# Kernel tuning notes

Measured on AMD Instinct MI355X. Metric: run time of the kernel, lower is better.

## Reference

```python
import jax, jax.numpy as jnp
import numpy as np

E = 1024      # embed_dim
H = 16        # num heads
D = E // H    # head_dim = 64
B, T = 4, 2048


def setup_inputs() -> dict:
    key = jax.random.key(0)
    ks = jax.random.split(key, 7)
    hidden_states = jax.random.normal(ks[0], (B, T, E), dtype=jnp.float32)
    # torch Linear weight layout: [out_features, in_features]
    Wqkv = jax.random.normal(ks[1], (3 * E, E), dtype=jnp.float32) * (1.0 / np.sqrt(E))
    bqkv = jax.random.normal(ks[2], (3 * E,), dtype=jnp.float32) * 0.02
    Wproj = jax.random.normal(ks[3], (E, E), dtype=jnp.float32) * (1.0 / np.sqrt(E))
    bproj = jax.random.normal(ks[4], (E,), dtype=jnp.float32) * 0.02
    splat_scale = jax.random.normal(ks[5], (H,), dtype=jnp.float32) * 0.5
    splat_bias = jax.random.normal(ks[6], (H, 1, 1), dtype=jnp.float32) * 0.5
    return {
        'hidden_states': hidden_states,
        'Wqkv': Wqkv, 'bqkv': bqkv,
        'Wproj': Wproj, 'bproj': bproj,
        'splat_scale': splat_scale, 'splat_bias': splat_bias,
    }


def reference(hidden_states, Wqkv, bqkv, Wproj, bproj, splat_scale, splat_bias):
    b, t, _ = hidden_states.shape
    scale_factor = 1.0 / np.sqrt(D)

    qkv = hidden_states @ Wqkv.T + bqkv                    # [B,T,3E]
    q, k, v = jnp.split(qkv, 3, axis=-1)
    # [B,H,T,D]
    q = q.reshape(b, t, H, D).transpose(0, 2, 1, 3)
    k = k.reshape(b, t, H, D).transpose(0, 2, 1, 3)
    v = v.reshape(b, t, H, D).transpose(0, 2, 1, 3)

    scores = jnp.einsum('bhqd,bhkd->bhqk', q * scale_factor, k)  # [B,H,T,T]

    s = (1.0 + 0.01 * jnp.tanh(splat_scale)).reshape(1, H, 1, 1)
    bsp = (0.001 * jnp.tanh(splat_bias)).reshape(1, H, 1, 1)
    scores = s * scores + bsp

    causal = jnp.tril(jnp.ones((t, t), dtype=bool))
    scores = jnp.where(causal, scores, jnp.float32(-1e9))

    attn = jax.nn.softmax(scores, axis=-1)                 # dropout = identity (eval)
    out = jnp.einsum('bhqk,bhkd->bhqd', attn, v)
    out = out.transpose(0, 2, 1, 3).reshape(b, t, E)
    out = out @ Wproj.T + bproj
    return out
```

## Files before the change

### kernel.cpp

```cpp
#include <hip/hip_runtime.h>
#include <stdint.h>

#define BB 4
#define TT 2048
#define EE 1024
#define HH 16
#define DD 64
#define MM (BB*TT)
#define NQKV (3*EE)

typedef __bf16 bf16_t;
typedef bf16_t bf16x8 __attribute__((ext_vector_type(8)));
typedef short  s16x4  __attribute__((ext_vector_type(4)));
typedef float  floatx4 __attribute__((ext_vector_type(4)));

__device__ __forceinline__ unsigned short f2bf(float f) {
    unsigned int u = __float_as_uint(f);
    u = (u + 0x7FFFu + ((u >> 16) & 1u)) >> 16;
    return (unsigned short)u;
}

__device__ __forceinline__ short bfs(float f) {
    return (short)__builtin_bit_cast(unsigned short, (bf16_t)f);
}

__device__ __forceinline__ void load_lds16(const void* g, void* l) {
    __builtin_amdgcn_global_load_lds(
        (const __attribute__((address_space(1))) unsigned int*)g,
        (__attribute__((address_space(3))) unsigned int*)l, 16, 0, 0);
}

__global__ void cvt_f32_bf16(const float* __restrict__ in,
                             unsigned short* __restrict__ out, int n) {
    int i = (blockIdx.x * 256 + threadIdx.x) * 4;
    if (i + 3 < n) {
        float4 v = *reinterpret_cast<const float4*>(in + i);
        ushort4 o;
        o.x = f2bf(v.x); o.y = f2bf(v.y); o.z = f2bf(v.z); o.w = f2bf(v.w);
        *reinterpret_cast<ushort4*>(out + i) = o;
    }
}

template<int N, int K, int EPI>
__global__ __launch_bounds__(256, 3) void gemm_bt(
    const unsigned short* __restrict__ A,
    const unsigned short* __restrict__ Bw,
    const float* __restrict__ bias,
    const float* __restrict__ sscale,
    unsigned short* __restrict__ Qb,
    unsigned short* __restrict__ Kb,
    unsigned short* __restrict__ Vtb,
    float* __restrict__ Cout)
{
    __shared__ __align__(16) unsigned short As[2][128 * 32];
    __shared__ __align__(16) unsigned short Bs[2][128 * 32];
    __shared__ float qsc[16];

    const int tid  = threadIdx.x;
    const int lane = tid & 63;
    const int w    = tid >> 6;
    const int quad = lane >> 4;
    const int l16  = lane & 15;
    const int m0   = blockIdx.y * 128;
    const int n0   = blockIdx.x * 128;
    const int wm   = (w & 1) * 64;
    const int wn   = (w >> 1) * 64;

    if (EPI == 0 && tid < 16) qsc[tid] = (1.0f + 0.01f * tanhf(sscale[tid])) * 0.125f;

    floatx4 acc[4][4] = {};

    const int rsl = (quad ^ ((l16 >> 1) & 3)) * 8;

    for (int kk = 0; kk < K; kk += 64) {
        __syncthreads();
#pragma unroll
        for (int h = 0; h < 2; ++h) {
#pragma unroll
            for (int c = 0; c < 2; ++c) {
                int idx = c * 256 + tid;
                int chk = (idx & 3) ^ ((idx >> 3) & 3);
                const unsigned short* ga = A  + (size_t)(m0 + (idx >> 2)) * K + kk + h * 32 + chk * 8;
                load_lds16(ga, &As[h][(c * 256 + w * 64) * 8]);
                const unsigned short* gb = Bw + (size_t)(n0 + (idx >> 2)) * K + kk + h * 32 + chk * 8;
                load_lds16(gb, &Bs[h][(c * 256 + w * 64) * 8]);
            }
        }
        __syncthreads();

#pragma unroll
        for (int h = 0; h < 2; ++h) {
            bf16x8 af[4], bfr[4];
#pragma unroll
            for (int mt = 0; mt < 4; ++mt)
                af[mt] = *reinterpret_cast<const bf16x8*>(&As[h][(wm + mt * 16 + l16) * 32 + rsl]);
#pragma unroll
            for (int nt = 0; nt < 4; ++nt)
                bfr[nt] = *reinterpret_cast<const bf16x8*>(&Bs[h][(wn + nt * 16 + l16) * 32 + rsl]);
#pragma unroll
            for (int mt = 0; mt < 4; ++mt)
#pragma unroll
                for (int nt = 0; nt < 4; ++nt)
                    acc[mt][nt] = __builtin_amdgcn_mfma_f32_16x16x32_bf16(af[mt], bfr[nt], acc[mt][nt], 0, 0, 0);
        }
    }

    if (EPI == 0) {
#pragma unroll
        for (int mt = 0; mt < 4; ++mt) {
            int rowb = m0 + wm + mt * 16 + quad * 4;
#pragma unroll
            for (int nt = 0; nt < 4; ++nt) {
                int col = n0 + wn + nt * 16 + l16;
                int which = col >> 10;
                int e = col & 1023;
                int h = e >> 6, d = e & 63;
                float bsv = bias[col];
#pragma unroll
                for (int r = 0; r < 4; ++r) {
                    int m = rowb + r;
                    int b = m >> 11, t = m & 2047;
                    float v = acc[mt][nt][r] + bsv;
                    size_t bh = (size_t)(b * HH + h);
                    if (which == 0) {
                        v *= qsc[h];
                        Qb[(bh * TT + t) * DD + d] = f2bf(v);
                    } else if (which == 1) {
                        Kb[(bh * TT + t) * DD + d] = f2bf(v);
                    } else {
                        Vtb[(bh * DD + d) * TT + t] = f2bf(v);
                    }
                }
            }
        }
    } else {
#pragma unroll
        for (int mt = 0; mt < 4; ++mt) {
            int rowb = m0 + wm + mt * 16 + quad * 4;
#pragma unroll
            for (int nt = 0; nt < 4; ++nt) {
                int col = n0 + wn + nt * 16 + l16;
                float bsv = bias[col];
#pragma unroll
                for (int r = 0; r < 4; ++r)
                    Cout[(size_t)(rowb + r) * N + col] = acc[mt][nt][r] + bsv;
            }
        }
    }
}

#define LP 72
__global__ __launch_bounds__(256, 4) void flash_attn(
    const unsigned short* __restrict__ Qb,
    const unsigned short* __restrict__ Kb,
    const unsigned short* __restrict__ Vtb,
    unsigned short* __restrict__ Ob)
{
    __shared__ __align__(16) unsigned short Ks[2][64 * LP];
    __shared__ __align__(16) unsigned short Vs[2][64 * LP];

    const int tid  = threadIdx.x;
    const int lane = tid & 63;
    const int w    = tid >> 6;
    const int quad = lane >> 4;
    const int l16  = lane & 15;
    const int i    = blockIdx.x;
    const int bh   = i & 63;
    const int qt   = 31 - (i >> 6);
    const int row0 = qt * 64 + w * 16;

    const unsigned short* qbase = &Qb[((size_t)bh * TT + row0 + l16) * DD + quad * 8];
    const bf16x8 qf0 = *reinterpret_cast<const bf16x8*>(qbase);
    const bf16x8 qf1 = *reinterpret_cast<const bf16x8*>(qbase + 32);

    const s16x4 vones = { (short)0x3F80, (short)0x3F80, (short)0x3F80, (short)0x3F80 };

    floatx4 o[4] = {};
    floatx4 o1 = {};

    const int srow = tid >> 3;
    const int scol = (tid & 7) * 8;
    const size_t kgbase = ((size_t)bh * TT + srow) * DD + scol;
    const size_t vgbase = ((size_t)bh * DD + srow) * TT + scol;

    uint4 kr0 = *reinterpret_cast<const uint4*>(&Kb[kgbase]);
    uint4 kr1 = *reinterpret_cast<const uint4*>(&Kb[kgbase + 32 * DD]);
    uint4 vr0 = *reinterpret_cast<const uint4*>(&Vtb[vgbase]);
    uint4 vr1 = *reinterpret_cast<const uint4*>(&Vtb[vgbase + 32 * TT]);

    for (int kt = 0; kt <= qt; ++kt) {
        const int buf = kt & 1;
        *reinterpret_cast<uint4*>(&Ks[buf][srow * LP + scol]) = kr0;
        *reinterpret_cast<uint4*>(&Ks[buf][(srow + 32) * LP + scol]) = kr1;
        *reinterpret_cast<uint4*>(&Vs[buf][srow * LP + scol]) = vr0;
        *reinterpret_cast<uint4*>(&Vs[buf][(srow + 32) * LP + scol]) = vr1;
        __syncthreads();

        if (kt < qt) {
            size_t ko = kgbase + (size_t)(kt + 1) * 64 * DD;
            size_t vo = vgbase + (size_t)(kt + 1) * 64;
            kr0 = *reinterpret_cast<const uint4*>(&Kb[ko]);
            kr1 = *reinterpret_cast<const uint4*>(&Kb[ko + 32 * DD]);
            vr0 = *reinterpret_cast<const uint4*>(&Vtb[vo]);
            vr1 = *reinterpret_cast<const uint4*>(&Vtb[vo + 32 * TT]);
        }

        const int keyb = kt * 64 + quad * 4;
        const int qr0  = row0 + l16;
        const bool diag = (kt == qt);

#pragma unroll
        for (int ntk = 0; ntk < 4; ++ntk) {
            const unsigned short* krow = &Ks[buf][(ntk * 16 + l16) * LP + quad * 8];
            bf16x8 kf0 = *reinterpret_cast<const bf16x8*>(krow);
            bf16x8 kf1 = *reinterpret_cast<const bf16x8*>(krow + 32);

            floatx4 st = {0.f, 0.f, 0.f, 0.f};
            st = __builtin_amdgcn_mfma_f32_16x16x32_bf16(kf0, qf0, st, 0, 0, 0);
            st = __builtin_amdgcn_mfma_f32_16x16x32_bf16(kf1, qf1, st, 0, 0, 0);

            float p0 = __expf(st[0]), p1 = __expf(st[1]);
            float p2 = __expf(st[2]), p3 = __expf(st[3]);
            if (diag) {
                const int kb = keyb + ntk * 16;
                p0 = (kb + 0 <= qr0) ? p0 : 0.f;
                p1 = (kb + 1 <= qr0) ? p1 : 0.f;
                p2 = (kb + 2 <= qr0) ? p2 : 0.f;
                p3 = (kb + 3 <= qr0) ? p3 : 0.f;
            }
            s16x4 pf;
            pf[0] = bfs(p0); pf[1] = bfs(p1); pf[2] = bfs(p2); pf[3] = bfs(p3);

            o1 = __builtin_amdgcn_mfma_f32_16x16x16bf16_1k(pf, vones, o1, 0, 0, 0);
#pragma unroll
            for (int dt = 0; dt < 4; ++dt) {
                s16x4 vf = *reinterpret_cast<const s16x4*>(
                    &Vs[buf][(dt * 16 + l16) * LP + ntk * 16 + quad * 4]);
                o[dt] = __builtin_amdgcn_mfma_f32_16x16x16bf16_1k(pf, vf, o[dt], 0, 0, 0);
            }
        }
    }

    const int b = bh >> 4, h = bh & 15;
#pragma unroll
    for (int r = 0; r < 4; ++r) {
        int q = row0 + quad * 4 + r;
        float rl = __builtin_amdgcn_rcpf(o1[r]);
#pragma unroll
        for (int dt = 0; dt < 4; ++dt)
            Ob[((size_t)(b * TT + q)) * EE + h * DD + dt * 16 + l16] =
                f2bf(o[dt][r] * rl);
    }
}

extern "C" void kernel_launch(void* const* d_in, const int* in_sizes, int n_in,
                              void* d_out, int out_size, void* d_ws, size_t ws_size,
                              hipStream_t stream) {
    const float* hs    = (const float*)d_in[0];
    const float* Wqkv  = (const float*)d_in[1];
    const float* bqkv  = (const float*)d_in[2];
    const float* Wproj = (const float*)d_in[3];
    const float* bproj = (const float*)d_in[4];
    const float* ss    = (const float*)d_in[5];
    float* out = (float*)d_out;

    char* p = (char*)d_ws;
    unsigned short* hsb    = (unsigned short*)p; p += (size_t)MM * EE * 2;
    unsigned short* wqkvb  = (unsigned short*)p; p += (size_t)NQKV * EE * 2;
    unsigned short* wprojb = (unsigned short*)p; p += (size_t)EE * EE * 2;
    unsigned short* Qb     = (unsigned short*)p; p += (size_t)BB*HH*TT*DD * 2;
    unsigned short* Kb     = (unsigned short*)p; p += (size_t)BB*HH*TT*DD * 2;
    unsigned short* Vtb    = (unsigned short*)p; p += (size_t)BB*HH*TT*DD * 2;

    cvt_f32_bf16<<<(MM * EE) / 1024, 256, 0, stream>>>(hs, hsb, MM * EE);
    cvt_f32_bf16<<<(NQKV * EE) / 1024, 256, 0, stream>>>(Wqkv, wqkvb, NQKV * EE);
    cvt_f32_bf16<<<(EE * EE) / 1024, 256, 0, stream>>>(Wproj, wprojb, EE * EE);

    gemm_bt<NQKV, EE, 0><<<dim3(NQKV / 128, MM / 128), 256, 0, stream>>>(
        hsb, wqkvb, bqkv, ss, Qb, Kb, Vtb, nullptr);

    flash_attn<<<dim3(2048), 256, 0, stream>>>(Qb, Kb, Vtb, hsb);

    gemm_bt<EE, EE, 1><<<dim3(EE / 128, MM / 128), 256, 0, stream>>>(
        hsb, wprojb, bproj, nullptr, nullptr, nullptr, nullptr, out);
}
```

Before: 276.3 us.

## Process two 64-row query groups per attention block to reuse K/V tiles

Each flash-attention block now handles 128 query rows, with each wave holding two 16-row query fragments, so every K/V tile loaded into shared memory serves twice as many queries. The grid is halved to 1024 blocks and a per-tile flag skips the first group's work past its diagonal. This cuts global K/V traffic and barrier count per query, at the cost of more accumulator registers (which may lower occupancy under the 256,4 launch bounds) and less causal load balance across blocks.

```diff
diff --git a/kernel.cpp b/kernel.cpp
--- a/kernel.cpp
+++ b/kernel.cpp
@@ -166,17 +166,19 @@
     const int l16  = lane & 15;
     const int i    = blockIdx.x;
     const int bh   = i & 63;
-    const int qt   = 31 - (i >> 6);
-    const int row0 = qt * 64 + w * 16;
+    const int qb   = 15 - (i >> 6);
+    const int row0 = qb * 128 + w * 16;
 
     const unsigned short* qbase = &Qb[((size_t)bh * TT + row0 + l16) * DD + quad * 8];
     const bf16x8 qf0 = *reinterpret_cast<const bf16x8*>(qbase);
     const bf16x8 qf1 = *reinterpret_cast<const bf16x8*>(qbase + 32);
+    const bf16x8 qg0 = *reinterpret_cast<const bf16x8*>(qbase + 64 * DD);
+    const bf16x8 qg1 = *reinterpret_cast<const bf16x8*>(qbase + 64 * DD + 32);
 
     const s16x4 vones = { (short)0x3F80, (short)0x3F80, (short)0x3F80, (short)0x3F80 };
 
-    floatx4 o[4] = {};
-    floatx4 o1 = {};
+    floatx4 o[4] = {}, ob[4] = {};
+    floatx4 o1 = {}, o1b = {};
 
     const int srow = tid >> 3;
     const int scol = (tid & 7) * 8;
@@ -188,7 +190,9 @@
     uint4 vr0 = *reinterpret_cast<const uint4*>(&Vtb[vgbase]);
     uint4 vr1 = *reinterpret_cast<const uint4*>(&Vtb[vgbase + 32 * TT]);
 
-    for (int kt = 0; kt <= qt; ++kt) {
+    const int ktmax = 2 * qb + 1;
+
+    for (int kt = 0; kt <= ktmax; ++kt) {
         const int buf = kt & 1;
         *reinterpret_cast<uint4*>(&Ks[buf][srow * LP + scol]) = kr0;
         *reinterpret_cast<uint4*>(&Ks[buf][(srow + 32) * LP + scol]) = kr1;
@@ -196,7 +200,7 @@
         *reinterpret_cast<uint4*>(&Vs[buf][(srow + 32) * LP + scol]) = vr1;
         __syncthreads();
 
-        if (kt < qt) {
+        if (kt < ktmax) {
             size_t ko = kgbase + (size_t)(kt + 1) * 64 * DD;
             size_t vo = vgbase + (size_t)(kt + 1) * 64;
             kr0 = *reinterpret_cast<const uint4*>(&Kb[ko]);
@@ -205,9 +209,11 @@
             vr1 = *reinterpret_cast<const uint4*>(&Vtb[vo + 32 * TT]);
         }
 
-        const int keyb = kt * 64 + quad * 4;
-        const int qr0  = row0 + l16;
-        const bool diag = (kt == qt);
+        const int keyb  = kt * 64 + quad * 4;
+        const int qr0   = row0 + l16;
+        const bool g0on = (kt <= 2 * qb);
+        const bool g0di = (kt == 2 * qb);
+        const bool g1di = (kt == ktmax);
 
 #pragma unroll
         for (int ntk = 0; ntk < 4; ++ntk) {
@@ -215,28 +221,45 @@
             bf16x8 kf0 = *reinterpret_cast<const bf16x8*>(krow);
             bf16x8 kf1 = *reinterpret_cast<const bf16x8*>(krow + 32);
 
-            floatx4 st = {0.f, 0.f, 0.f, 0.f};
-            st = __builtin_amdgcn_mfma_f32_16x16x32_bf16(kf0, qf0, st, 0, 0, 0);
-            st = __builtin_amdgcn_mfma_f32_16x16x32_bf16(kf1, qf1, st, 0, 0, 0);
-
-            float p0 = __expf(st[0]), p1 = __expf(st[1]);
-            float p2 = __expf(st[2]), p3 = __expf(st[3]);
-            if (diag) {
-                const int kb = keyb + ntk * 16;
-                p0 = (kb + 0 <= qr0) ? p0 : 0.f;
-                p1 = (kb + 1 <= qr0) ? p1 : 0.f;
-                p2 = (kb + 2 <= qr0) ? p2 : 0.f;
-                p3 = (kb + 3 <= qr0) ? p3 : 0.f;
-            }
-            s16x4 pf;
-            pf[0] = bfs(p0); pf[1] = bfs(p1); pf[2] = bfs(p2); pf[3] = bfs(p3);
-
-            o1 = __builtin_amdgcn_mfma_f32_16x16x16bf16_1k(pf, vones, o1, 0, 0, 0);
+            s16x4 pf, pfb;
+            if (g0on) {
+                floatx4 st = {0.f, 0.f, 0.f, 0.f};
+                st = __builtin_amdgcn_mfma_f32_16x16x32_bf16(kf0, qf0, st, 0, 0, 0);
+                st = __builtin_amdgcn_mfma_f32_16x16x32_bf16(kf1, qf1, st, 0, 0, 0);
+                float p0 = __expf(st[0]), p1 = __expf(st[1]);
+                float p2 = __expf(st[2]), p3 = __expf(st[3]);
+                if (g0di) {
+                    const int kb = keyb + ntk * 16;
+                    p0 = (kb + 0 <= qr0) ? p0 : 0.f;
+                    p1 = (kb + 1 <= qr0) ? p1 : 0.f;
+                    p2 = (kb + 2 <= qr0) ? p2 : 0.f;
+                    p3 = (kb + 3 <= qr0) ? p3 : 0.f;
+                }
+                pf[0] = bfs(p0); pf[1] = bfs(p1); pf[2] = bfs(p2); pf[3] = bfs(p3);
+                o1 = __builtin_amdgcn_mfma_f32_16x16x16bf16_1k(pf, vones, o1, 0, 0, 0);
+            }
+            {
+                floatx4 st = {0.f, 0.f, 0.f, 0.f};
+                st = __builtin_amdgcn_mfma_f32_16x16x32_bf16(kf0, qg0, st, 0, 0, 0);
+                st = __builtin_amdgcn_mfma_f32_16x16x32_bf16(kf1, qg1, st, 0, 0, 0);
+                float p0 = __expf(st[0]), p1 = __expf(st[1]);
+                float p2 = __expf(st[2]), p3 = __expf(st[3]);
+                if (g1di) {
+                    const int kb = keyb + ntk * 16, qr1 = qr0 + 64;
+                    p0 = (kb + 0 <= qr1) ? p0 : 0.f;
+                    p1 = (kb + 1 <= qr1) ? p1 : 0.f;
+                    p2 = (kb + 2 <= qr1) ? p2 : 0.f;
+                    p3 = (kb + 3 <= qr1) ? p3 : 0.f;
+                }
+                pfb[0] = bfs(p0); pfb[1] = bfs(p1); pfb[2] = bfs(p2); pfb[3] = bfs(p3);
+                o1b = __builtin_amdgcn_mfma_f32_16x16x16bf16_1k(pfb, vones, o1b, 0, 0, 0);
+            }
 #pragma unroll
             for (int dt = 0; dt < 4; ++dt) {
                 s16x4 vf = *reinterpret_cast<const s16x4*>(
                     &Vs[buf][(dt * 16 + l16) * LP + ntk * 16 + quad * 4]);
-                o[dt] = __builtin_amdgcn_mfma_f32_16x16x16bf16_1k(pf, vf, o[dt], 0, 0, 0);
+                if (g0on) o[dt] = __builtin_amdgcn_mfma_f32_16x16x16bf16_1k(pf, vf, o[dt], 0, 0, 0);
+                ob[dt] = __builtin_amdgcn_mfma_f32_16x16x16bf16_1k(pfb, vf, ob[dt], 0, 0, 0);
             }
         }
     }
@@ -244,12 +267,16 @@
     const int b = bh >> 4, h = bh & 15;
 #pragma unroll
     for (int r = 0; r < 4; ++r) {
-        int q = row0 + quad * 4 + r;
-        float rl = __builtin_amdgcn_rcpf(o1[r]);
-#pragma unroll
-        for (int dt = 0; dt < 4; ++dt)
-            Ob[((size_t)(b * TT + q)) * EE + h * DD + dt * 16 + l16] =
-                f2bf(o[dt][r] * rl);
+        int q0 = row0 + quad * 4 + r;
+        float rl0 = __builtin_amdgcn_rcpf(o1[r]);
+        float rl1 = __builtin_amdgcn_rcpf(o1b[r]);
+#pragma unroll
+        for (int dt = 0; dt < 4; ++dt) {
+            Ob[((size_t)(b * TT + q0)) * EE + h * DD + dt * 16 + l16] =
+                f2bf(o[dt][r] * rl0);
+            Ob[((size_t)(b * TT + q0 + 64)) * EE + h * DD + dt * 16 + l16] =
+                f2bf(ob[dt][r] * rl1);
+        }
     }
 }
 
@@ -279,7 +306,7 @@
     gemm_bt<NQKV, EE, 0><<<dim3(NQKV / 128, MM / 128), 256, 0, stream>>>(
         hsb, wqkvb, bqkv, ss, Qb, Kb, Vtb, nullptr);
 
-    flash_attn<<<dim3(2048), 256, 0, stream>>>(Qb, Kb, Vtb, hsb);
+    flash_attn<<<dim3(1024), 256, 0, stream>>>(Qb, Kb, Vtb, hsb);
 
     gemm_bt<EE, EE, 1><<<dim3(EE / 128, MM / 128), 256, 0, stream>>>(
         hsb, wprojb, bproj, nullptr, nullptr, nullptr, nullptr, out);
```

Measured after the change: 468.6 us. 1.7x slower.
